# Kernel optimization log

Hardware: AMD Instinct MI355X
Metric: run time of the kernel (lower is better)

Reference implementation:

```python
import jax, jax.numpy as jnp
import numpy as np

L = 3          # num_layers
H = 128        # hidden_dim
NH = 4         # num heads
DH = H // NH   # head dim
B = 32         # graphs per batch
N = 1024       # nodes per graph
NTOT = B * N
DEG = 16
E = NTOT * DEG
BN_EPS = 1e-5


def setup_inputs() -> dict:
    key = jax.random.key(0)
    ks = jax.random.split(key, 16)
    s = 1.0 / np.sqrt(H)
    inp = {
        "x": jax.random.normal(ks[0], (NTOT, H), jnp.float32),
        "edge_attr": jax.random.normal(ks[1], (E, H), jnp.float32),
        "gine_w1": jax.random.normal(ks[2], (L, H, H), jnp.float32) * s,
        "gine_b1": jnp.zeros((L, H), jnp.float32),
        "gine_bn_g": jnp.ones((L, H), jnp.float32),
        "gine_bn_b": jnp.zeros((L, H), jnp.float32),
        "gine_w2": jax.random.normal(ks[3], (L, H, H), jnp.float32) * s,
        "gine_b2": jnp.zeros((L, H), jnp.float32),
        "attn_wqkv": jax.random.normal(ks[4], (L, 3 * H, H), jnp.float32) * s,
        "attn_bqkv": jnp.zeros((L, 3 * H), jnp.float32),
        "attn_wo": jax.random.normal(ks[5], (L, H, H), jnp.float32) * s,
        "attn_bo": jnp.zeros((L, H), jnp.float32),
        "norm1_g": jnp.ones((L, H), jnp.float32),
        "norm1_b": jnp.zeros((L, H), jnp.float32),
        "norm2_g": jnp.ones((L, H), jnp.float32),
        "norm2_b": jnp.zeros((L, H), jnp.float32),
        "norm3_g": jnp.ones((L, H), jnp.float32),
        "norm3_b": jnp.zeros((L, H), jnp.float32),
        "mlp_w1": jax.random.normal(ks[6], (L, 2 * H, H), jnp.float32) * s,
        "mlp_b1": jnp.zeros((L, 2 * H), jnp.float32),
        "mlp_w2": jax.random.normal(ks[7], (L, H, 2 * H), jnp.float32) * (1.0 / np.sqrt(2 * H)),
        "mlp_b2": jnp.zeros((L, H), jnp.float32),
    }
    # intra-graph random edges: local src/dst in [0, N) plus per-graph offset
    offs = (jnp.arange(E, dtype=jnp.int32) // (N * DEG)) * N  # graph offset per edge
    src = jax.random.randint(ks[8], (E,), 0, N, jnp.int32) + offs
    dst = jax.random.randint(ks[9], (E,), 0, N, jnp.int32) + offs
    inp["edge_index"] = jnp.stack([src, dst]).astype(jnp.int32)
    inp["batch"] = (jnp.arange(NTOT, dtype=jnp.int32) // N)
    return inp


def _bn(x, g, b):
    m = x.mean(axis=0)
    v = jnp.var(x, axis=0)
    return (x - m) * jax.lax.rsqrt(v + BN_EPS) * g + b


def _gps_forward(x, edge_attr, gine_w1, gine_b1, gine_bn_g, gine_bn_b, gine_w2, gine_b2,
                 attn_wqkv, attn_bqkv, attn_wo, attn_bo,
                 norm1_g, norm1_b, norm2_g, norm2_b, norm3_g, norm3_b,
                 mlp_w1, mlp_b1, mlp_w2, mlp_b2, edge_index, batch):
    src, dst = edge_index[0], edge_index[1]
    for i in range(L):
        # ---- GINEConv: msg = relu(x_j + e), sum-scatter, nn-MLP on x + aggr (eps=0)
        msg = jax.nn.relu(x[src] + edge_attr)                       # [E, H]
        aggr = jax.ops.segment_sum(msg, dst, num_segments=NTOT)     # [NTOT, H]
        h = x + aggr
        h = h @ gine_w1[i].T + gine_b1[i]
        h = jax.nn.relu(_bn(h, gine_bn_g[i], gine_bn_b[i]))
        h = h @ gine_w2[i].T + gine_b2[i]
        h_local = _bn(h + x, norm1_g[i], norm1_b[i])                # residual + norm1
        # ---- global multi-head attention on x (dense per-graph, equal sizes)
        xb = x.reshape(B, N, H)
        qkv = xb @ attn_wqkv[i].T + attn_bqkv[i]                    # [B, N, 3H]
        q, k, v = jnp.split(qkv, 3, axis=-1)
        q = q.reshape(B, N, NH, DH).transpose(0, 2, 1, 3)           # [B, nh, N, dh]
        k = k.reshape(B, N, NH, DH).transpose(0, 2, 1, 3)
        v = v.reshape(B, N, NH, DH).transpose(0, 2, 1, 3)
        scores = jnp.einsum("bhqd,bhkd->bhqk", q, k) / np.sqrt(DH)
        attn = jax.nn.softmax(scores, axis=-1)
        o = jnp.einsum("bhqk,bhkd->bhqd", attn, v)
        o = o.transpose(0, 2, 1, 3).reshape(B, N, H) @ attn_wo[i].T + attn_bo[i]
        h_attn = _bn(o.reshape(NTOT, H) + x, norm2_g[i], norm2_b[i])
        # ---- combine + FFN + norm3
        out = h_local + h_attn
        ff = jax.nn.relu(out @ mlp_w1[i].T + mlp_b1[i]) @ mlp_w2[i].T + mlp_b2[i]
        x = _bn(out + ff, norm3_g[i], norm3_b[i])
        if i != L - 1:
            x = jax.nn.relu(x)
    return x


def reference(x, edge_attr, gine_w1, gine_b1, gine_bn_g, gine_bn_b, gine_w2, gine_b2,
              attn_wqkv, attn_bqkv, attn_wo, attn_bo,
              norm1_g, norm1_b, norm2_g, norm2_b, norm3_g, norm3_b,
              mlp_w1, mlp_b1, mlp_w2, mlp_b2, edge_index, batch):
    return _gps_forward(x, edge_attr, gine_w1, gine_b1, gine_bn_g, gine_bn_b, gine_w2, gine_b2,
                        attn_wqkv, attn_bqkv, attn_wo, attn_bo,
                        norm1_g, norm1_b, norm2_g, norm2_b, norm3_g, norm3_b,
                        mlp_w1, mlp_b1, mlp_w2, mlp_b2, edge_index, batch)
```

## Files before the change

kernel.cpp:

```cpp
#include <hip/hip_runtime.h>
#include <hip/hip_bf16.h>
#include <math.h>

#define NTOT 32768
#define HDIM 128
#define NE   524288
#define NGRAPH 32
#define NNODE 1024
#define NHEAD 4
#define DHEAD 32

typedef __attribute__((ext_vector_type(8))) short bf8v;
typedef __attribute__((ext_vector_type(4))) float f4v;
typedef unsigned short u16;

__device__ __forceinline__ float4 ld4(const float* p){ return *(const float4*)p; }

__device__ __forceinline__ u16 bf16rn(float f){
  union { float f; unsigned u; } x; x.f = f;
  unsigned r = x.u + 0x7FFF + ((x.u >> 16) & 1);
  return (u16)(r >> 16);
}
__device__ __forceinline__ unsigned pk2(float a, float b){
  unsigned r;
  asm("v_cvt_pk_bf16_f32 %0, %1, %2" : "=v"(r) : "v"(a), "v"(b));
  return r;
}
__device__ __forceinline__ float bf2f(u16 u){
  union { unsigned u; float f; } x; x.u = ((unsigned)u) << 16;
  return x.f;
}

__global__ void k_count(const int* __restrict__ dst, int* __restrict__ deg){
  int e = blockIdx.x*256 + threadIdx.x;
  atomicAdd(&deg[dst[e]], 1);
}

__global__ __launch_bounds__(1024) void k_scan(const int* __restrict__ deg,
                                               int* __restrict__ indptr,
                                               int* __restrict__ cursor){
  __shared__ int sm[1024];
  int t = threadIdx.x;
  int base = t*32;
  int s = 0;
  for (int j=0;j<32;j++) s += deg[base+j];
  sm[t] = s; __syncthreads();
  for (int off=1; off<1024; off<<=1){
    int v = (t>=off) ? sm[t-off] : 0;
    __syncthreads();
    sm[t] += v;
    __syncthreads();
  }
  int ex = sm[t] - s;
  for (int j=0;j<32;j++){
    int d = deg[base+j];
    indptr[base+j] = ex; cursor[base+j] = ex;
    ex += d;
  }
  if (t == 1023) indptr[NTOT] = ex;
}

__global__ void k_fill(const int* __restrict__ dst, int* __restrict__ cursor,
                       int* __restrict__ epos){
  int e = blockIdx.x*256 + threadIdx.x;
  int pos = atomicAdd(&cursor[dst[e]], 1);
  epos[e] = pos;
}

__global__ __launch_bounds__(256) void k_prep(const float* __restrict__ ea,
    const int* __restrict__ src, const int* __restrict__ epos,
    u16* __restrict__ EAb, int* __restrict__ SRCp,
    const float* __restrict__ x, u16* __restrict__ Xb,
    const float* s0,const float* s1,const float* s2,
    const float* s3,const float* s4,const float* s5, u16* __restrict__ Wb){
  int b = blockIdx.x, tid = threadIdx.x;
  if (b < 65536){
    int e = b*8 + (tid>>5);
    int c4 = (tid&31)*4;
    int pos = epos[e];
    float4 v = ld4(&ea[(size_t)e*HDIM + c4]);
    uint2 o; o.x = pk2(v.x, v.y); o.y = pk2(v.z, v.w);
    *(uint2*)&EAb[(size_t)pos*HDIM + c4] = o;
    if ((tid&31) == 0) SRCp[pos] = src[e];
  } else if (b < 69632){
    size_t i = ((size_t)(b-65536)*256 + tid)*4;
    float4 v = ld4(&x[i]);
    uint2 o; o.x = pk2(v.x,v.y); o.y = pk2(v.z,v.w);
    *(uint2*)&Xb[i] = o;
  } else {
    int idx = b - 69632;
    int y = idx / 144;
    int i = (idx % 144)*256 + tid;
    const float* srcs[6] = {s0,s1,s2,s3,s4,s5};
    const int cnt4[6] = {12288,12288,36864,12288,24576,24576};
    const int off[6]  = {0,49152,98304,245760,294912,393216};
    if (i < cnt4[y]){
      float4 v = ld4(&srcs[y][(size_t)i*4]);
      uint2 o; o.x = pk2(v.x,v.y); o.y = pk2(v.z,v.w);
      *(uint2*)&Wb[off[y] + (size_t)i*4] = o;
    }
  }
}

__device__ __forceinline__ void aggr_body(int bx, int tid,
    const u16* __restrict__ Xb, const u16* __restrict__ EAb,
    const int* __restrict__ SRCp, const int* __restrict__ indptr,
    u16* __restrict__ Hb){
  int n = bx*8 + (tid>>5);
  int c4 = (tid&31)*4;
  int p0 = indptr[n], p1 = indptr[n+1];
  float a0=0.f,a1=0.f,a2=0.f,a3=0.f;
  int p = p0;
  int sNext = (p < p1) ? SRCp[p] : 0;
  for (; p<p1; p++){
    int s = sNext;
    if (p+1 < p1) sNext = SRCp[p+1];
    uint2 ev = *(const uint2*)&EAb[(size_t)p*HDIM + c4];
    uint2 xv = *(const uint2*)&Xb[(size_t)s*HDIM + c4];
    a0 += fmaxf(bf2f((u16)(xv.x&0xffff)) + bf2f((u16)(ev.x&0xffff)), 0.f);
    a1 += fmaxf(bf2f((u16)(xv.x>>16))    + bf2f((u16)(ev.x>>16)), 0.f);
    a2 += fmaxf(bf2f((u16)(xv.y&0xffff)) + bf2f((u16)(ev.y&0xffff)), 0.f);
    a3 += fmaxf(bf2f((u16)(xv.y>>16))    + bf2f((u16)(ev.y>>16)), 0.f);
  }
  uint2 xn = *(const uint2*)&Xb[(size_t)n*HDIM + c4];
  a0 += bf2f((u16)(xn.x&0xffff)); a1 += bf2f((u16)(xn.x>>16));
  a2 += bf2f((u16)(xn.y&0xffff)); a3 += bf2f((u16)(xn.y>>16));
  uint2 o; o.x = pk2(a0,a1); o.y = pk2(a2,a3);
  *(uint2*)&Hb[(size_t)n*HDIM + c4] = o;
}

template<bool BNA, bool DUAL, bool RELU, bool EP, bool STATS, bool WROUT>
__device__ __forceinline__ void bgemm_body(int bx, int by, int tid,
    const u16* __restrict__ Ab, const u16* __restrict__ A2b,
    const float* __restrict__ slotA, const float* __restrict__ gA, const float* __restrict__ bA,
    const float* __restrict__ slotB, const float* __restrict__ gB, const float* __restrict__ bB,
    const u16* __restrict__ Wb, const float* __restrict__ bias,
    const u16* __restrict__ Epb, u16* __restrict__ Cb,
    u16* __restrict__ OUTb, float* __restrict__ slotOut, int N, int K,
    float* sbn1, float* sbn2, float* sred){
  int w = tid>>6, l = tid&63;
  int q = l&15, g = l>>4;
  int m0 = bx*128, n0 = by*64;
  int wr = w*32;
  const float invn = 1.0f/32768.0f;
  if ((BNA || DUAL) && tid < 128){
    float mean = slotA[tid]*invn;
    float var  = slotA[128+tid]*invn - mean*mean;
    float s = gA[tid] * rsqrtf(var + 1e-5f);
    sbn1[tid] = s; sbn1[128+tid] = bA[tid] - mean*s;
    if (DUAL){
      float mean2 = slotB[tid]*invn;
      float var2  = slotB[128+tid]*invn - mean2*mean2;
      float s2 = gB[tid] * rsqrtf(var2 + 1e-5f);
      sbn2[tid] = s2; sbn2[128+tid] = bB[tid] - mean2*s2;
    }
  }
  if (STATS && tid < 128) sred[tid] = 0.f;
  if (BNA || DUAL || STATS) __syncthreads();

  f4v acc[2][4];
  #pragma unroll
  for (int i=0;i<2;i++)
    #pragma unroll
    for (int j=0;j<4;j++) acc[i][j] = (f4v){0.f,0.f,0.f,0.f};

  for (int kc=0; kc<K; kc+=32){
    bf8v af[2];
    #pragma unroll
    for (int mt=0;mt<2;mt++){
      int row = m0 + wr + 16*mt + q;
      if (!BNA && !DUAL){
        af[mt] = *(const bf8v*)&Ab[(size_t)row*K + kc + 8*g];
      } else {
        union { bf8v b; u16 s[8]; unsigned u[4]; } ra, r2, ro;
        ra.b = *(const bf8v*)&Ab[(size_t)row*K + kc + 8*g];
        if (DUAL) r2.b = *(const bf8v*)&A2b[(size_t)row*K + kc + 8*g];
        float v[8];
        #pragma unroll
        for (int j=0;j<8;j++){
          int kk = kc + 8*g + j;
          float f = bf2f(ra.s[j]) * sbn1[kk] + sbn1[128+kk];
          if (BNA) f = fmaxf(f, 0.f);
          if (DUAL) f += bf2f(r2.s[j]) * sbn2[kk] + sbn2[128+kk];
          v[j] = f;
        }
        ro.u[0]=pk2(v[0],v[1]); ro.u[1]=pk2(v[2],v[3]);
        ro.u[2]=pk2(v[4],v[5]); ro.u[3]=pk2(v[6],v[7]);
        af[mt] = ro.b;
        if (WROUT && by == 0)
          *(uint4*)&OUTb[(size_t)row*K + kc + 8*g] = *(uint4*)ro.u;
      }
    }
    bf8v bfv[4];
    #pragma unroll
    for (int nt=0;nt<4;nt++)
      bfv[nt] = *(const bf8v*)&Wb[(size_t)(n0+16*nt+q)*K + kc + 8*g];
    #pragma unroll
    for (int mt=0;mt<2;mt++)
      #pragma unroll
      for (int nt=0;nt<4;nt++)
        acc[mt][nt] = __builtin_amdgcn_mfma_f32_16x16x32_bf16(af[mt], bfv[nt], acc[mt][nt], 0,0,0);
  }
  float bbv[4];
  #pragma unroll
  for (int nt=0;nt<4;nt++) bbv[nt] = bias[n0 + 16*nt + q];
  float csum[4] = {0.f,0.f,0.f,0.f}, csq[4] = {0.f,0.f,0.f,0.f};
  #pragma unroll
  for (int mt=0;mt<2;mt++){
    int row0 = m0 + wr + 16*mt + 4*g;
    #pragma unroll
    for (int nt=0;nt<4;nt++){
      int col = n0 + 16*nt + q;
      #pragma unroll
      for (int r=0;r<4;r++){
        size_t off = (size_t)(row0+r)*N + col;
        float v = acc[mt][nt][r] + bbv[nt];
        if (EP) v += bf2f(Epb[off]);
        if (RELU) v = fmaxf(v, 0.f);
        Cb[off] = bf16rn(v);
        if (STATS){ csum[nt] += v; csq[nt] += v*v; }
      }
    }
  }
  if (STATS){
    #pragma unroll
    for (int nt=0;nt<4;nt++){
      int c = 16*nt + q;
      atomicAdd(&sred[c], csum[nt]);
      atomicAdd(&sred[64+c], csq[nt]);
    }
    __syncthreads();
    if (tid < 64){
      atomicAdd(&slotOut[n0+tid], sred[tid]);
      atomicAdd(&slotOut[128+n0+tid], sred[64+tid]);
    }
  }
}

__device__ __forceinline__ void qkv_body(int bx, int by, int tid,
    const u16* __restrict__ Ab, const u16* __restrict__ Wb, const float* __restrict__ bias,
    u16* __restrict__ Qb, u16* __restrict__ Kb, u16* __restrict__ VT, u16* Sm){
  int w = tid>>6, l = tid&63;
  int q = l&15, g = l>>4;
  int which = by >> 1, half = by & 1;
  int m0 = bx*128, n0 = by*64;
  const int K = 128;
  int wr = w*32;
  f4v acc[2][4];
  #pragma unroll
  for (int i=0;i<2;i++)
    #pragma unroll
    for (int j=0;j<4;j++) acc[i][j] = (f4v){0.f,0.f,0.f,0.f};
  for (int kc=0; kc<K; kc+=32){
    bf8v af[2];
    #pragma unroll
    for (int mt=0;mt<2;mt++)
      af[mt] = *(const bf8v*)&Ab[(size_t)(m0+wr+16*mt+q)*K + kc + 8*g];
    bf8v bfv[4];
    #pragma unroll
    for (int nt=0;nt<4;nt++)
      bfv[nt] = *(const bf8v*)&Wb[(size_t)(n0+16*nt+q)*K + kc + 8*g];
    #pragma unroll
    for (int mt=0;mt<2;mt++)
      #pragma unroll
      for (int nt=0;nt<4;nt++)
        acc[mt][nt] = __builtin_amdgcn_mfma_f32_16x16x32_bf16(af[mt], bfv[nt], acc[mt][nt], 0,0,0);
  }
  const float QSC = 0.17677669529663687f * 1.4426950408889634f;
  float scale = (which==0) ? QSC : 1.0f;
  float bbv[4];
  #pragma unroll
  for (int nt=0;nt<4;nt++) bbv[nt] = bias[n0 + 16*nt + q];
  if (which < 2){
    #pragma unroll
    for (int mt=0;mt<2;mt++){
      int row0 = wr + 16*mt + 4*g;
      #pragma unroll
      for (int nt=0;nt<4;nt++){
        int c = 16*nt + q;
        #pragma unroll
        for (int r=0;r<4;r++)
          Sm[(row0+r)*72 + c] = bf16rn((acc[mt][nt][r] + bbv[nt]) * scale);
      }
    }
    __syncthreads();
    u16* dst = (which==0) ? Qb : Kb;
    #pragma unroll
    for (int it=0; it<4; it++){
      int idx = tid + it*256;
      int row = idx >> 3, c8 = (idx & 7) * 8;
      uint4 v = *(const uint4*)&Sm[row*72 + c8];
      *(uint4*)&dst[(size_t)(m0+row)*128 + half*64 + c8] = v;
    }
  } else {
    #pragma unroll
    for (int mt=0;mt<2;mt++){
      int row0 = wr + 16*mt + 4*g;
      #pragma unroll
      for (int nt=0;nt<4;nt++){
        int c = 16*nt + q;
        uint2 p;
        p.x = pk2(acc[mt][nt][0] + bbv[nt], acc[mt][nt][1] + bbv[nt]);
        p.y = pk2(acc[mt][nt][2] + bbv[nt], acc[mt][nt][3] + bbv[nt]);
        *(uint2*)&Sm[c*136 + row0] = p;
      }
    }
    __syncthreads();
    int gg = m0 >> 10;
    int nl0 = m0 & 1023;
    #pragma unroll
    for (int it=0; it<4; it++){
      int idx = tid + it*256;
      int c = idx >> 4, n8 = (idx & 15) * 8;
      uint4 v = *(const uint4*)&Sm[c*136 + n8];
      *(uint4*)&VT[((size_t)gg*128 + half*64 + c)*1024 + nl0 + n8] = v;
    }
  }
}

__device__ __forceinline__ void flash_body(int qt, int h, int g, int tid,
    const u16* __restrict__ Qb, const u16* __restrict__ Kb, const u16* __restrict__ VT,
    u16* __restrict__ O, u16* Pl){
  int w = tid >> 6, l = tid & 63;
  int q = l & 15, grp = l >> 4;
  size_t gbase = (size_t)g*1024;
  size_t qrow0 = gbase + qt*64 + w*16;
  const u16* Vp = VT + ((size_t)(g*4 + h)*32)*1024;
  bf8v qf = *(const bf8v*)&Qb[(qrow0 + q)*128 + h*32 + 8*grp];
  u16* Pw = Pl + w*(16*72);
  float m = -1e30f, lsum = 0.f;
  f4v o0 = {0.f,0.f,0.f,0.f}, o1 = {0.f,0.f,0.f,0.f};
  for (int kt=0; kt<16; kt++){
    int k0 = kt*64;
    f4v st[4];
    #pragma unroll
    for (int t=0;t<4;t++){
      bf8v kf = *(const bf8v*)&Kb[(gbase + k0 + 16*t + q)*128 + h*32 + 8*grp];
      st[t] = __builtin_amdgcn_mfma_f32_16x16x32_bf16(kf, qf, (f4v){0.f,0.f,0.f,0.f}, 0,0,0);
    }
    float smax = st[0][0];
    #pragma unroll
    for (int t=0;t<4;t++)
      #pragma unroll
      for (int r=0;r<4;r++) smax = fmaxf(smax, st[t][r]);
    smax = fmaxf(smax, __shfl_xor(smax, 16));
    smax = fmaxf(smax, __shfl_xor(smax, 32));
    float mnew = fmaxf(m, smax);
    float alpha = exp2f(m - mnew);
    float psum = 0.f;
    #pragma unroll
    for (int t=0;t<4;t++){
      float p0 = exp2f(st[t][0]-mnew), p1 = exp2f(st[t][1]-mnew);
      float p2 = exp2f(st[t][2]-mnew), p3 = exp2f(st[t][3]-mnew);
      psum += (p0+p1)+(p2+p3);
      *(unsigned*)&Pw[q*72 + 16*t + 4*grp]     = pk2(p0,p1);
      *(unsigned*)&Pw[q*72 + 16*t + 4*grp + 2] = pk2(p2,p3);
    }
    psum += __shfl_xor(psum, 16);
    psum += __shfl_xor(psum, 32);
    lsum = lsum*alpha + psum;
    m = mnew;
    f4v aD;
    #pragma unroll
    for (int r=0;r<4;r++) aD[r] = __shfl(alpha, 4*grp + r);
    #pragma unroll
    for (int r=0;r<4;r++){ o0[r] *= aD[r]; o1[r] *= aD[r]; }
    bf8v pa0 = *(const bf8v*)&Pw[q*72 + 8*grp];
    bf8v pa1 = *(const bf8v*)&Pw[q*72 + 32 + 8*grp];
    bf8v v00 = *(const bf8v*)&Vp[(size_t)q*1024      + k0 + 8*grp];
    bf8v v01 = *(const bf8v*)&Vp[(size_t)q*1024      + k0 + 32 + 8*grp];
    bf8v v10 = *(const bf8v*)&Vp[(size_t)(16+q)*1024 + k0 + 8*grp];
    bf8v v11 = *(const bf8v*)&Vp[(size_t)(16+q)*1024 + k0 + 32 + 8*grp];
    o0 = __builtin_amdgcn_mfma_f32_16x16x32_bf16(pa0, v00, o0, 0,0,0);
    o0 = __builtin_amdgcn_mfma_f32_16x16x32_bf16(pa1, v01, o0, 0,0,0);
    o1 = __builtin_amdgcn_mfma_f32_16x16x32_bf16(pa0, v10, o1, 0,0,0);
    o1 = __builtin_amdgcn_mfma_f32_16x16x32_bf16(pa1, v11, o1, 0,0,0);
  }
  f4v lD;
  #pragma unroll
  for (int r=0;r<4;r++) lD[r] = __shfl(lsum, 4*grp + r);
  #pragma unroll
  for (int r=0;r<4;r++){
    float inv = 1.0f/lD[r];
    size_t row = qrow0 + 4*grp + r;
    O[row*HDIM + h*32 + q]      = bf16rn(o0[r]*inv);
    O[row*HDIM + h*32 + 16 + q] = bf16rn(o1[r]*inv);
  }
}

__global__ __launch_bounds__(256) void k_d1(const u16* __restrict__ Xb,
    const u16* __restrict__ EAb, const int* __restrict__ SRCp, const int* __restrict__ indptr,
    u16* __restrict__ Hb,
    const u16* __restrict__ wq, const float* __restrict__ BQ,
    u16* __restrict__ Qb, u16* __restrict__ Kb, u16* __restrict__ VTb){
  __shared__ u16 Sm[128*72];
  int bx = blockIdx.x;
  if (bx < 4096){
    aggr_body(bx, threadIdx.x, Xb, EAb, SRCp, indptr, Hb);
  } else {
    int b = bx - 4096;
    qkv_body(b & 255, b >> 8, threadIdx.x, Xb, wq, BQ, Qb, Kb, VTb, Sm);
  }
}

__global__ __launch_bounds__(256) void k_d2(const u16* __restrict__ Qb,
    const u16* __restrict__ Kb, const u16* __restrict__ VTb, u16* __restrict__ Ob,
    const u16* __restrict__ Hb, const u16* __restrict__ w1, const float* __restrict__ B1,
    u16* __restrict__ G1, float* __restrict__ S0){
  __shared__ u16 Pl[4*16*72];
  __shared__ float sb1[256], sb2[256], sr[128];
  int bx = blockIdx.x;
  if (bx < 2048){
    flash_body(bx & 15, (bx >> 4) & 3, bx >> 6, threadIdx.x, Qb, Kb, VTb, Ob, Pl);
  } else {
    int b = bx - 2048;
    bgemm_body<false,false,false,false,true,false>(b & 255, b >> 8, threadIdx.x,
      Hb, nullptr, nullptr,nullptr,nullptr, nullptr,nullptr,nullptr,
      w1, B1, nullptr, G1, nullptr, S0, 128, 128, sb1, sb2, sr);
  }
}

__global__ __launch_bounds__(256) void k_d3(const u16* __restrict__ G1,
    const float* __restrict__ S0, const float* __restrict__ bnG, const float* __restrict__ bnB,
    const u16* __restrict__ w2, const float* __restrict__ B2,
    const u16* __restrict__ Xb, u16* __restrict__ P1, float* __restrict__ S1,
    const u16* __restrict__ Ob, const u16* __restrict__ wo, const float* __restrict__ BO,
    u16* __restrict__ P2, float* __restrict__ S2){
  __shared__ float sb1[256], sb2[256], sr[128];
  int bx = blockIdx.x;
  if (bx < 512){
    bgemm_body<true,false,false,true,true,false>(bx & 255, bx >> 8, threadIdx.x,
      G1, nullptr, S0, bnG, bnB, nullptr,nullptr,nullptr,
      w2, B2, Xb, P1, nullptr, S1, 128, 128, sb1, sb2, sr);
  } else {
    int b = bx - 512;
    bgemm_body<false,false,false,true,true,false>(b & 255, b >> 8, threadIdx.x,
      Ob, nullptr, nullptr,nullptr,nullptr, nullptr,nullptr,nullptr,
      wo, BO, Xb, P2, nullptr, S2, 128, 128, sb1, sb2, sr);
  }
}

__global__ __launch_bounds__(256) void k_mlp1(const u16* __restrict__ P1, const u16* __restrict__ P2,
    const float* __restrict__ S1, const float* __restrict__ n1g, const float* __restrict__ n1b,
    const float* __restrict__ S2, const float* __restrict__ n2g, const float* __restrict__ n2b,
    const u16* __restrict__ wm1, const float* __restrict__ BM1,
    u16* __restrict__ FFb, u16* __restrict__ OUTb){
  __shared__ float sb1[256], sb2[256], sr[128];
  bgemm_body<false,true,true,false,false,true>(blockIdx.x, blockIdx.y, threadIdx.x,
    P1, P2, S1, n1g, n1b, S2, n2g, n2b,
    wm1, BM1, nullptr, FFb, OUTb, nullptr, 256, 128, sb1, sb2, sr);
}

__global__ __launch_bounds__(256) void k_mlp2(const u16* __restrict__ FFb,
    const u16* __restrict__ wm2, const float* __restrict__ BM2,
    const u16* __restrict__ OUTb, u16* __restrict__ H3, float* __restrict__ S3){
  __shared__ float sb1[256], sb2[256], sr[128];
  bgemm_body<false,false,false,true,true,false>(blockIdx.x, blockIdx.y, threadIdx.x,
    FFb, nullptr, nullptr,nullptr,nullptr, nullptr,nullptr,nullptr,
    wm2, BM2, OUTb, H3, nullptr, S3, 128, 256, sb1, sb2, sr);
}

template<bool RELU, bool F32OUT>
__global__ __launch_bounds__(256) void k_bnapply(const u16* __restrict__ X,
    const float* __restrict__ slot, const float* __restrict__ gv, const float* __restrict__ bv,
    u16* __restrict__ Yb, float* __restrict__ Yf){
  int idx = blockIdx.x*256 + threadIdx.x;
  int row = idx >> 4, c8 = (idx & 15) * 8;
  const float invn = 1.0f/32768.0f;
  union { uint4 u; u16 s[8]; } iv;
  iv.u = *(const uint4*)&X[(size_t)row*HDIM + c8];
  float o[8];
  #pragma unroll
  for (int j=0;j<8;j++){
    int c = c8+j;
    float mean = slot[c]*invn;
    float var  = slot[128+c]*invn - mean*mean;
    float sc = gv[c] * rsqrtf(var + 1e-5f);
    float sh = bv[c] - mean*sc;
    float v = bf2f(iv.s[j])*sc + sh;
    if (RELU) v = fmaxf(v, 0.f);
    o[j] = v;
  }
  if (F32OUT){
    float* dst = &Yf[(size_t)row*HDIM + c8];
    *(float4*)dst = make_float4(o[0],o[1],o[2],o[3]);
    *(float4*)(dst+4) = make_float4(o[4],o[5],o[6],o[7]);
  } else {
    uint4 ov;
    ov.x = pk2(o[0],o[1]); ov.y = pk2(o[2],o[3]);
    ov.z = pk2(o[4],o[5]); ov.w = pk2(o[6],o[7]);
    *(uint4*)&Yb[(size_t)row*HDIM + c8] = ov;
  }
}

extern "C" void kernel_launch(void* const* d_in, const int* in_sizes, int n_in,
                              void* d_out, int out_size, void* d_ws, size_t ws_size,
                              hipStream_t stream){
  const float* x_in      = (const float*)d_in[0];
  const float* edge_attr = (const float*)d_in[1];
  const float* gine_w1   = (const float*)d_in[2];
  const float* gine_b1   = (const float*)d_in[3];
  const float* gine_bn_g = (const float*)d_in[4];
  const float* gine_bn_b = (const float*)d_in[5];
  const float* gine_w2   = (const float*)d_in[6];
  const float* gine_b2   = (const float*)d_in[7];
  const float* attn_wqkv = (const float*)d_in[8];
  const float* attn_bqkv = (const float*)d_in[9];
  const float* attn_wo   = (const float*)d_in[10];
  const float* attn_bo   = (const float*)d_in[11];
  const float* norm1_g   = (const float*)d_in[12];
  const float* norm1_b   = (const float*)d_in[13];
  const float* norm2_g   = (const float*)d_in[14];
  const float* norm2_b   = (const float*)d_in[15];
  const float* norm3_g   = (const float*)d_in[16];
  const float* norm3_b   = (const float*)d_in[17];
  const float* mlp_w1    = (const float*)d_in[18];
  const float* mlp_b1    = (const float*)d_in[19];
  const float* mlp_w2    = (const float*)d_in[20];
  const float* mlp_b2    = (const float*)d_in[21];
  const int* edge_index  = (const int*)d_in[22];
  const int* srcp = edge_index;
  const int* dstp = edge_index + NE;
  float* out = (float*)d_out;

  float* ws = (float*)d_ws;
  const size_t U = 4194304;
  u16* Xb   = (u16*)(ws);
  u16* Hb   = (u16*)(ws + U/2);
  u16* G1   = (u16*)(ws + U);
  u16* P1   = (u16*)(ws + U + U/2);
  u16* P2   = (u16*)(ws + 2*U);
  u16* Ob   = (u16*)(ws + 2*U + U/2);
  u16* FFb  = (u16*)(ws + 3*U);
  u16* OUTb = (u16*)(ws + 4*U);
  u16* H3   = (u16*)(ws + 4*U + U/2);
  u16* Qb   = (u16*)(ws + 5*U);
  u16* Kb   = (u16*)(ws + 5*U + U/2);
  u16* VTb  = (u16*)(ws + 6*U);
  u16* Wball= (u16*)(ws + 6*U + U/2);
  float* STATS = ws + 7*U - 8192;
  int* IW      = (int*)(ws + 7*U);
  int* deg     = IW;
  int* indptr  = IW + 32768;
  int* cursor  = IW + 32768 + 32772;
  int* epos    = cursor + 32768;
  u16* EAb  = (u16*)(ws + 8*U);
  int* SRCp = (int*)(ws + 16*U);

  u16* W1b  = Wball + 0;
  u16* W2b  = Wball + 49152;
  u16* WQb  = Wball + 98304;
  u16* WOb  = Wball + 245760;
  u16* WM1b = Wball + 294912;
  u16* WM2b = Wball + 393216;

  hipMemsetAsync(STATS, 0, 8192*sizeof(float) + NTOT*sizeof(int), stream);
  k_count<<<NE/256, 256, 0, stream>>>(dstp, deg);
  k_scan<<<1, 1024, 0, stream>>>(deg, indptr, cursor);
  k_fill<<<NE/256, 256, 0, stream>>>(dstp, cursor, epos);
  k_prep<<<70496, 256, 0, stream>>>(edge_attr, srcp, epos, EAb, SRCp, x_in, Xb,
                                    gine_w1, gine_w2, attn_wqkv, attn_wo, mlp_w1, mlp_w2, Wball);

  for (int i=0;i<3;i++){
    const float* B1 = gine_b1 + (size_t)i*HDIM;
    const float* B2 = gine_b2 + (size_t)i*HDIM;
    const float* BQ = attn_bqkv + (size_t)i*3*HDIM;
    const float* BO = attn_bo + (size_t)i*HDIM;
    const float* BM1 = mlp_b1 + (size_t)i*2*HDIM;
    const float* BM2 = mlp_b2 + (size_t)i*HDIM;
    u16* w1 = W1b + (size_t)i*16384;
    u16* w2 = W2b + (size_t)i*16384;
    u16* wq = WQb + (size_t)i*49152;
    u16* wo = WOb + (size_t)i*16384;
    u16* wm1 = WM1b + (size_t)i*32768;
    u16* wm2 = WM2b + (size_t)i*32768;
    float* S0 = STATS + (size_t)(i*4+0)*512;
    float* S1 = STATS + (size_t)(i*4+1)*512;
    float* S2 = STATS + (size_t)(i*4+2)*512;
    float* S3 = STATS + (size_t)(i*4+3)*512;
    const float* bnG = gine_bn_g + (size_t)i*HDIM;
    const float* bnB = gine_bn_b + (size_t)i*HDIM;
    const float* n1g = norm1_g + (size_t)i*HDIM, *n1b = norm1_b + (size_t)i*HDIM;
    const float* n2g = norm2_g + (size_t)i*HDIM, *n2b = norm2_b + (size_t)i*HDIM;
    const float* n3g = norm3_g + (size_t)i*HDIM, *n3b = norm3_b + (size_t)i*HDIM;

    k_d1<<<5632, 256, 0, stream>>>(Xb, EAb, SRCp, indptr, Hb, wq, BQ, Qb, Kb, VTb);
    k_d2<<<2560, 256, 0, stream>>>(Qb, Kb, VTb, Ob, Hb, w1, B1, G1, S0);
    k_d3<<<1024, 256, 0, stream>>>(G1, S0, bnG, bnB, w2, B2, Xb, P1, S1,
                                   Ob, wo, BO, P2, S2);
    k_mlp1<<<dim3(256,4), 256, 0, stream>>>(P1, P2, S1, n1g, n1b, S2, n2g, n2b,
                                            wm1, BM1, FFb, OUTb);
    k_mlp2<<<dim3(256,2), 256, 0, stream>>>(FFb, wm2, BM2, OUTb, H3, S3);

    if (i<2) k_bnapply<true ,false><<<2048, 256, 0, stream>>>(H3, S3, n3g, n3b, Xb, nullptr);
    else     k_bnapply<false,true ><<<2048, 256, 0, stream>>>(H3, S3, n3g, n3b, nullptr, out);
  }
}
```

Measured before the change: 982.4 us.

## Fuse MLP GEMMs into one kernel and skip small softmax rescales

Merges the two FFN GEMM kernels into one kernel per 64-row tile. The ReLU hidden activations and the combined residual input stay in shared memory instead of making a round trip through global memory, and one launch is removed. Separately, the flash-attention loop now keeps the running max unchanged unless some lane's new max exceeds it by more than 8 (log2 units), which skips the exp and accumulator rescale in most iterations. The skip stays numerically safe because exponents are bounded by 2^8. The fused kernel uses a lot of LDS and registers (acc1 has 16 f4v), and its 512 blocks may leave the GPU with low occupancy.

```diff
diff --git a/kernel.cpp b/kernel.cpp
--- a/kernel.cpp
+++ b/kernel.cpp
@@ -345,8 +345,12 @@
       for (int r=0;r<4;r++) smax = fmaxf(smax, st[t][r]);
     smax = fmaxf(smax, __shfl_xor(smax, 16));
     smax = fmaxf(smax, __shfl_xor(smax, 32));
-    float mnew = fmaxf(m, smax);
-    float alpha = exp2f(m - mnew);
+    bool need = __any(smax > m + 8.f);
+    float mnew = m, alpha = 1.f;
+    if (need){
+      mnew = fmaxf(m, smax);
+      alpha = exp2f(m - mnew);
+    }
     float psum = 0.f;
     #pragma unroll
     for (int t=0;t<4;t++){
@@ -360,11 +364,13 @@
     psum += __shfl_xor(psum, 32);
     lsum = lsum*alpha + psum;
     m = mnew;
-    f4v aD;
-    #pragma unroll
-    for (int r=0;r<4;r++) aD[r] = __shfl(alpha, 4*grp + r);
-    #pragma unroll
-    for (int r=0;r<4;r++){ o0[r] *= aD[r]; o1[r] *= aD[r]; }
+    if (need){
+      f4v aD;
+      #pragma unroll
+      for (int r=0;r<4;r++) aD[r] = __shfl(alpha, 4*grp + r);
+      #pragma unroll
+      for (int r=0;r<4;r++){ o0[r] *= aD[r]; o1[r] *= aD[r]; }
+    }
     bf8v pa0 = *(const bf8v*)&Pw[q*72 + 8*grp];
     bf8v pa1 = *(const bf8v*)&Pw[q*72 + 32 + 8*grp];
     bf8v v00 = *(const bf8v*)&Vp[(size_t)q*1024      + k0 + 8*grp];
@@ -440,24 +446,106 @@
   }
 }
 
-__global__ __launch_bounds__(256) void k_mlp1(const u16* __restrict__ P1, const u16* __restrict__ P2,
+__global__ __launch_bounds__(256) void k_mlpf(const u16* __restrict__ P1, const u16* __restrict__ P2,
     const float* __restrict__ S1, const float* __restrict__ n1g, const float* __restrict__ n1b,
     const float* __restrict__ S2, const float* __restrict__ n2g, const float* __restrict__ n2b,
     const u16* __restrict__ wm1, const float* __restrict__ BM1,
-    u16* __restrict__ FFb, u16* __restrict__ OUTb){
-  __shared__ float sb1[256], sb2[256], sr[128];
-  bgemm_body<false,true,true,false,false,true>(blockIdx.x, blockIdx.y, threadIdx.x,
-    P1, P2, S1, n1g, n1b, S2, n2g, n2b,
-    wm1, BM1, nullptr, FFb, OUTb, nullptr, 256, 128, sb1, sb2, sr);
-}
-
-__global__ __launch_bounds__(256) void k_mlp2(const u16* __restrict__ FFb,
     const u16* __restrict__ wm2, const float* __restrict__ BM2,
-    const u16* __restrict__ OUTb, u16* __restrict__ H3, float* __restrict__ S3){
-  __shared__ float sb1[256], sb2[256], sr[128];
-  bgemm_body<false,false,false,true,true,false>(blockIdx.x, blockIdx.y, threadIdx.x,
-    FFb, nullptr, nullptr,nullptr,nullptr, nullptr,nullptr,nullptr,
-    wm2, BM2, OUTb, H3, nullptr, S3, 128, 256, sb1, sb2, sr);
+    u16* __restrict__ H3, float* __restrict__ S3){
+  __shared__ u16 FF[64][268];
+  __shared__ u16 OUTs[64][138];
+  __shared__ float sb1[256], sb2[256], sred[256];
+  int tid = threadIdx.x;
+  int w = tid>>6, l = tid&63;
+  int q = l&15, g = l>>4;
+  int m0 = blockIdx.x*64;
+  const float invn = 1.0f/32768.0f;
+  if (tid < 128){
+    float mean = S1[tid]*invn;
+    float var  = S1[128+tid]*invn - mean*mean;
+    float s = n1g[tid] * rsqrtf(var + 1e-5f);
+    sb1[tid] = s; sb1[128+tid] = n1b[tid] - mean*s;
+    float mean2 = S2[tid]*invn;
+    float var2  = S2[128+tid]*invn - mean2*mean2;
+    float s2 = n2g[tid] * rsqrtf(var2 + 1e-5f);
+    sb2[tid] = s2; sb2[128+tid] = n2b[tid] - mean2*s2;
+    sred[tid] = 0.f; sred[128+tid] = 0.f;
+  }
+  __syncthreads();
+
+  f4v acc1[16];
+  #pragma unroll
+  for (int j=0;j<16;j++) acc1[j] = (f4v){0.f,0.f,0.f,0.f};
+  int lrow = w*16 + q;
+  int row = m0 + lrow;
+  for (int kc=0; kc<128; kc+=32){
+    union { bf8v b; u16 s[8]; unsigned u[4]; } ra, r2, ro;
+    ra.b = *(const bf8v*)&P1[(size_t)row*128 + kc + 8*g];
+    r2.b = *(const bf8v*)&P2[(size_t)row*128 + kc + 8*g];
+    float v[8];
+    #pragma unroll
+    for (int j=0;j<8;j++){
+      int kk = kc + 8*g + j;
+      v[j] = bf2f(ra.s[j]) * sb1[kk] + sb1[128+kk]
+           + bf2f(r2.s[j]) * sb2[kk] + sb2[128+kk];
+    }
+    ro.u[0]=pk2(v[0],v[1]); ro.u[1]=pk2(v[2],v[3]);
+    ro.u[2]=pk2(v[4],v[5]); ro.u[3]=pk2(v[6],v[7]);
+    *(uint4*)&OUTs[lrow][kc + 8*g] = *(uint4*)ro.u;
+    #pragma unroll
+    for (int nt=0;nt<16;nt++){
+      bf8v bv = *(const bf8v*)&wm1[(size_t)(16*nt+q)*128 + kc + 8*g];
+      acc1[nt] = __builtin_amdgcn_mfma_f32_16x16x32_bf16(ro.b, bv, acc1[nt], 0,0,0);
+    }
+  }
+  #pragma unroll
+  for (int nt=0;nt<16;nt++){
+    int col = 16*nt + q;
+    float bb = BM1[col];
+    int r0 = w*16 + 4*g;
+    #pragma unroll
+    for (int r=0;r<4;r++)
+      FF[r0+r][col] = bf16rn(fmaxf(acc1[nt][r] + bb, 0.f));
+  }
+  __syncthreads();
+
+  f4v acc2[8];
+  #pragma unroll
+  for (int j=0;j<8;j++) acc2[j] = (f4v){0.f,0.f,0.f,0.f};
+  for (int kc=0; kc<256; kc+=32){
+    bf8v af = *(const bf8v*)&FF[lrow][kc + 8*g];
+    #pragma unroll
+    for (int nt=0;nt<8;nt++){
+      bf8v bv = *(const bf8v*)&wm2[(size_t)(16*nt+q)*256 + kc + 8*g];
+      acc2[nt] = __builtin_amdgcn_mfma_f32_16x16x32_bf16(af, bv, acc2[nt], 0,0,0);
+    }
+  }
+  float csum[8], csq[8];
+  #pragma unroll
+  for (int nt=0;nt<8;nt++){ csum[nt]=0.f; csq[nt]=0.f; }
+  int r0 = w*16 + 4*g;
+  #pragma unroll
+  for (int nt=0;nt<8;nt++){
+    int col = 16*nt + q;
+    float bb = BM2[col];
+    #pragma unroll
+    for (int r=0;r<4;r++){
+      float v = acc2[nt][r] + bb + bf2f(OUTs[r0+r][col]);
+      H3[(size_t)(m0+r0+r)*128 + col] = bf16rn(v);
+      csum[nt] += v; csq[nt] += v*v;
+    }
+  }
+  #pragma unroll
+  for (int nt=0;nt<8;nt++){
+    int c = 16*nt + q;
+    atomicAdd(&sred[c], csum[nt]);
+    atomicAdd(&sred[128+c], csq[nt]);
+  }
+  __syncthreads();
+  if (tid < 128){
+    atomicAdd(&S3[tid], sred[tid]);
+    atomicAdd(&S3[128+tid], sred[128+tid]);
+  }
 }
 
 template<bool RELU, bool F32OUT>
@@ -531,9 +619,7 @@
   u16* P1   = (u16*)(ws + U + U/2);
   u16* P2   = (u16*)(ws + 2*U);
   u16* Ob   = (u16*)(ws + 2*U + U/2);
-  u16* FFb  = (u16*)(ws + 3*U);
-  u16* OUTb = (u16*)(ws + 4*U);
-  u16* H3   = (u16*)(ws + 4*U + U/2);
+  u16* H3   = (u16*)(ws + 3*U);
   u16* Qb   = (u16*)(ws + 5*U);
   u16* Kb   = (u16*)(ws + 5*U + U/2);
   u16* VTb  = (u16*)(ws + 6*U);
@@ -588,9 +674,8 @@
     k_d2<<<2560, 256, 0, stream>>>(Qb, Kb, VTb, Ob, Hb, w1, B1, G1, S0);
     k_d3<<<1024, 256, 0, stream>>>(G1, S0, bnG, bnB, w2, B2, Xb, P1, S1,
                                    Ob, wo, BO, P2, S2);
-    k_mlp1<<<dim3(256,4), 256, 0, stream>>>(P1, P2, S1, n1g, n1b, S2, n2g, n2b,
-                                            wm1, BM1, FFb, OUTb);
-    k_mlp2<<<dim3(256,2), 256, 0, stream>>>(FFb, wm2, BM2, OUTb, H3, S3);
+    k_mlpf<<<512, 256, 0, stream>>>(P1, P2, S1, n1g, n1b, S2, n2g, n2b,
+                                    wm1, BM1, wm2, BM2, H3, S3);
 
     if (i<2) k_bnapply<true ,false><<<2048, 256, 0, stream>>>(H3, S3, n3g, n3b, Xb, nullptr);
     else     k_bnapply<false,true ><<<2048, 256, 0, stream>>>(H3, S3, n3g, n3b, nullptr, out);
```

After: 979.0 us (median of 2 runs). About the same (-0.3%).
